# Kernel tuning notes

Hardware: AMD Instinct MI355X
Metric: run time of the kernel (lower is better)

## Reference

```python
import jax, jax.numpy as jnp
import numpy as np

GROUPS = 12
POOL = 64
TOPK = 8
LAYERS = 24
RANK = 64
HID = 1024


def setup_inputs() -> dict:
    key = jax.random.key(0)
    k1, k2, k3 = jax.random.split(key, 3)
    queries = jax.random.normal(k1, (64, 768), dtype=jnp.float32)
    keys = jax.random.normal(k2, (1, GROUPS, POOL, 768 // GROUPS), dtype=jnp.float32)
    weight_offset = jax.random.normal(
        k3, (POOL, 2, HID * RANK * LAYERS), dtype=jnp.float32
    )
    return {"queries": queries, "keys": keys, "weight_offset": weight_offset}


def reference(queries, keys, weight_offset):
    # queries: [b, g*c] -> [b, g, c]
    b = queries.shape[0]
    q = queries.reshape(b, GROUPS, -1)
    # cosine similarity against pool keys: sim [b, g, pool]
    qn = q / jnp.clip(jnp.linalg.norm(q, axis=-1, keepdims=True), 1e-8)
    kn = keys[0] / jnp.clip(jnp.linalg.norm(keys[0], axis=-1, keepdims=True), 1e-8)
    sim = jnp.einsum("bgc,gpc->bgp", qn, kn)
    # routing uses detached similarities (sim.clone().detach())
    idx_sim = jax.lax.stop_gradient(sim)
    # use_distance_weight=True path: mean over batch and groups -> [pool]
    mean_sim = jnp.mean(idx_sim, axis=(0, 1))
    dis_weight, idx_vote = jax.lax.top_k(mean_sim, TOPK)
    dis_weight = dis_weight / (dis_weight.sum() + 1e-9)
    # gather top-k low-rank factors: [k, 2, D]
    wo = weight_offset[idx_vote]
    low_rank_a = wo[:, 0, :].reshape(TOPK, LAYERS, RANK, HID)
    low_rank_b = wo[:, 1, :].reshape(TOPK, LAYERS, RANK, HID)
    # [k, L, H, H] low-rank outer products
    offset = jnp.einsum("nlrx,nlry->nlxy", low_rank_a, low_rank_b)
    # distance-weighted combine -> [L, H, H]
    weight_offset_out = jnp.einsum("n,nlxy->lxy", dis_weight, offset)
    return weight_offset_out
```

## Files before the change

### kernel.cpp

```cpp
#include <hip/hip_runtime.h>
#include <hip/hip_bf16.h>

#define GROUPS 12
#define POOL   64
#define TOPK   8
#define LAYERS 24
#define RANK   64
#define HID    1024
#define D_LR   (HID * RANK * LAYERS)
#define POOL_STRIDE (2L * D_LR)

typedef __attribute__((ext_vector_type(8))) short bf16x8;
typedef __attribute__((ext_vector_type(4))) float f32x4;

__device__ __forceinline__ unsigned bfpack2(float lo, float hi) {
    float2 t; t.x = lo; t.y = hi;
    union { __hip_bfloat162 h; unsigned u; } cv;
    cv.h = __float22bfloat162_rn(t);
    return cv.u;
}

__device__ __forceinline__ int sw_idx(int col, int chunk) {
    return chunk ^ (col & 7) ^ ((col >> 2) & 7);
}

__global__ void routing_kernel(const float* __restrict__ q,
                               const float* __restrict__ keys,
                               int* __restrict__ idx_out,
                               float* __restrict__ w_out) {
    __shared__ float invn[64][GROUPS];
    __shared__ float qbar[GROUPS][64];
    __shared__ float simg[GROUPS][64];
    const int t = threadIdx.x;

    {
        int b = t / GROUPS, g = t % GROUPS;
        const float* row = q + b * 768 + g * 64;
        float ss = 0.f;
        #pragma unroll 8
        for (int c = 0; c < 64; ++c) { float v = row[c]; ss = fmaf(v, v, ss); }
        invn[b][g] = 1.f / fmaxf(sqrtf(ss), 1e-8f);
    }
    __syncthreads();
    {
        int g = t >> 6, c = t & 63;
        float s = 0.f;
        for (int b = 0; b < 64; ++b) s = fmaf(q[b * 768 + g * 64 + c], invn[b][g], s);
        qbar[g][c] = s;
    }
    __syncthreads();
    {
        int g = t >> 6, p = t & 63;
        const float* krow = keys + (g * 64 + p) * 64;
        float ss = 0.f, dot = 0.f;
        #pragma unroll 8
        for (int c = 0; c < 64; ++c) {
            float v = krow[c];
            ss  = fmaf(v, v, ss);
            dot = fmaf(v, qbar[g][c], dot);
        }
        simg[g][p] = dot / fmaxf(sqrtf(ss), 1e-8f);
    }
    __syncthreads();
    if (t < 64) {
        float s = 0.f;
        for (int g = 0; g < GROUPS; ++g) s += simg[g][t];
        qbar[0][t] = s * (1.f / 768.f);
    }
    __syncthreads();
    if (t == 0) {
        float ms[POOL];
        for (int p = 0; p < POOL; ++p) ms[p] = qbar[0][p];
        float sum = 0.f;
        float vals[TOPK]; int ids[TOPK];
        for (int k = 0; k < TOPK; ++k) {
            float best = -3.4e38f; int bi = 0;
            for (int p = 0; p < POOL; ++p)
                if (ms[p] > best) { best = ms[p]; bi = p; }
            vals[k] = best; ids[k] = bi;
            ms[bi] = -3.4e38f; sum += best;
        }
        float inv = 1.f / (sum + 1e-9f);
        for (int k = 0; k < TOPK; ++k) { idx_out[k] = ids[k]; w_out[k] = vals[k] * inv; }
    }
}

__global__ __launch_bounds__(512, 2) void lowrank_mfma_kernel(
        const float* __restrict__ wo,
        const int*   __restrict__ idx,
        const float* __restrict__ w,
        float*       __restrict__ out)
{
    __shared__ uint4 As4[256][8];
    __shared__ uint4 Bs4[256][8];
    __shared__ int   s_idx[TOPK];
    __shared__ float s_w[TOPK];

    const int tid = threadIdx.x;
    const int b   = blockIdx.x;
    const int xcd = b & 7;
    const int i   = b >> 3;

    const int tile0 = (2 * xcd + (i >> 4)) * 16 + (i & 15);
    const int nt    = (i < 16) ? 2 : 1;
    const int tile1 = (16 + xcd) * 16 + i;

    if (tid < TOPK) { s_idx[tid] = idx[tid]; s_w[tid] = w[tid]; }
    __syncthreads();

    const int lane = tid & 63;
    const int wave = tid >> 6;
    const int wr = wave >> 2;
    const int wc = wave & 3;
    const int fr = lane & 15;
    const int kb = lane >> 4;

    const int c4 = lane;
    const int rg = wave;

    f32x4 acc[8][4];
    #pragma unroll
    for (int p = 0; p < 8; ++p)
        #pragma unroll
        for (int q2 = 0; q2 < 4; ++q2) acc[p][q2] = (f32x4){0.f, 0.f, 0.f, 0.f};

    f32x4 araw[8], braw[8];

    auto load_raw = [&](int T, int s) {
        const int l   = T >> 4;
        const int rem = T & 15;
        const int m0  = (rem >> 2) * 256;
        const int n0  = (rem & 3) * 256;
        const long base = (long)s_idx[s] * POOL_STRIDE + (long)l * (RANK * HID);
        const float* pa = wo + base + (long)(rg * 8) * HID + (m0 + c4 * 4);
        const float* pb = wo + base + D_LR + (long)(rg * 8) * HID + (n0 + c4 * 4);
        #pragma unroll
        for (int j = 0; j < 8; ++j) araw[j] = *(const f32x4*)(pa + (long)j * HID);
        #pragma unroll
        for (int j = 0; j < 8; ++j) braw[j] = *(const f32x4*)(pb + (long)j * HID);
    };

    load_raw(tile0, 0);

    for (int ti = 0; ti < nt; ++ti) {
        const int T   = (ti == 0) ? tile0 : tile1;
        const int l   = T >> 4;
        const int rem = T & 15;
        const int m0  = (rem >> 2) * 256;
        const int n0  = (rem & 3) * 256;

        for (int s = 0; s < 8; ++s) {
            const float wn = s_w[s];
            #pragma unroll
            for (int cc = 0; cc < 4; ++cc) {
                const int col = c4 * 4 + cc;
                uint4 ua, ub;
                ua.x = bfpack2(wn * araw[0][cc], wn * araw[1][cc]);
                ua.y = bfpack2(wn * araw[2][cc], wn * araw[3][cc]);
                ua.z = bfpack2(wn * araw[4][cc], wn * araw[5][cc]);
                ua.w = bfpack2(wn * araw[6][cc], wn * araw[7][cc]);
                ub.x = bfpack2(braw[0][cc], braw[1][cc]);
                ub.y = bfpack2(braw[2][cc], braw[3][cc]);
                ub.z = bfpack2(braw[4][cc], braw[5][cc]);
                ub.w = bfpack2(braw[6][cc], braw[7][cc]);
                const int cp = sw_idx(col, rg);
                As4[col][cp] = ua;
                Bs4[col][cp] = ub;
            }
            __syncthreads();

            if (s < 7)            load_raw(T, s + 1);
            else if (ti + 1 < nt) load_raw(tile1, 0);

            #pragma unroll
            for (int kk = 0; kk < 2; ++kk) {
                const int chunk = kk * 4 + kb;
                bf16x8 bfv[4];
                #pragma unroll
                for (int fj = 0; fj < 4; ++fj) {
                    const int n = wc * 64 + fj * 16 + fr;
                    bfv[fj] = *(const bf16x8*)&Bs4[n][sw_idx(n, chunk)];
                }
                #pragma unroll
                for (int fi = 0; fi < 8; ++fi) {
                    const int m = wr * 128 + fi * 16 + fr;
                    const bf16x8 af = *(const bf16x8*)&As4[m][sw_idx(m, chunk)];
                    #pragma unroll
                    for (int fj = 0; fj < 4; ++fj)
                        acc[fi][fj] = __builtin_amdgcn_mfma_f32_16x16x32_bf16(
                            af, bfv[fj], acc[fi][fj], 0, 0, 0);
                }
            }
            __syncthreads();
        }

        float* o = out + (long)l * (1024 * 1024);
        #pragma unroll
        for (int fi = 0; fi < 8; ++fi) {
            #pragma unroll
            for (int fj = 0; fj < 4; ++fj) {
                const int n = n0 + wc * 64 + fj * 16 + fr;
                #pragma unroll
                for (int v = 0; v < 4; ++v) {
                    const int m = m0 + wr * 128 + fi * 16 + kb * 4 + v;
                    o[(long)m * 1024 + n] = acc[fi][fj][v];
                }
                acc[fi][fj] = (f32x4){0.f, 0.f, 0.f, 0.f};
            }
        }
    }
}

extern "C" void kernel_launch(void* const* d_in, const int* in_sizes, int n_in,
                              void* d_out, int out_size, void* d_ws, size_t ws_size,
                              hipStream_t stream) {
    const float* q    = (const float*)d_in[0];
    const float* keys = (const float*)d_in[1];
    const float* wo   = (const float*)d_in[2];
    float* out = (float*)d_out;

    int*   idx = (int*)d_ws;
    float* w   = (float*)((char*)d_ws + 32);

    routing_kernel<<<1, 768, 0, stream>>>(q, keys, idx, w);

    lowrank_mfma_kernel<<<dim3(256, 1, 1), 512, 0, stream>>>(wo, idx, w, out);
}
```

Baseline: 80.14 us.

## Pre-convert selected low-rank factors to swizzled bf16 panels, stream via LDS loads

Adds a separate convert kernel that gathers the top-k factor slices, applies the distance weight, converts them to bf16 and writes them to a workspace in a pre-swizzled panel layout. The GEMM kernel then copies those panels straight into double-buffered LDS with global_load_lds, so the per-tile fp32 loads and register conversion are gone and the next stage's loads overlap the MFMA work. The cost is an extra kernel launch and a workspace round-trip of the bf16 panels. The new path depends on the workspace being large enough; otherwise it falls back to the old kernel.

```diff
diff --git a/kernel.cpp b/kernel.cpp
--- a/kernel.cpp
+++ b/kernel.cpp
@@ -9,6 +9,8 @@
 #define HID    1024
 #define D_LR   (HID * RANK * LAYERS)
 #define POOL_STRIDE (2L * D_LR)
+#define PAN_U4 8192
+#define WS_PAN_BYTES ((size_t)LAYERS * TOPK * 2 * PAN_U4 * 16)
 
 typedef __attribute__((ext_vector_type(8))) short bf16x8;
 typedef __attribute__((ext_vector_type(4))) float f32x4;
@@ -22,6 +24,12 @@
 
 __device__ __forceinline__ int sw_idx(int col, int chunk) {
     return chunk ^ (col & 7) ^ ((col >> 2) & 7);
+}
+
+__device__ __forceinline__ void gll16(const void* g, void* l) {
+    __builtin_amdgcn_global_load_lds(
+        (const __attribute__((address_space(1))) unsigned*)g,
+        (__attribute__((address_space(3))) unsigned*)l, 16, 0, 0);
 }
 
 __global__ void routing_kernel(const float* __restrict__ q,
@@ -85,16 +93,40 @@
     }
 }
 
-__global__ __launch_bounds__(512, 2) void lowrank_mfma_kernel(
-        const float* __restrict__ wo,
-        const int*   __restrict__ idx,
-        const float* __restrict__ w,
+__global__ __launch_bounds__(256) void convert_kernel(
+        const float* __restrict__ wo, const int* __restrict__ idx,
+        const float* __restrict__ w, uint4* __restrict__ pan) {
+    const int bid = blockIdx.x;
+    const int mat = bid & 1;
+    const int s   = (bid >> 1) & 7;
+    const int cb  = (bid >> 4) & 3;
+    const int l   = bid >> 6;
+    const int tid = threadIdx.x;
+    const int col = cb * 256 + tid;
+    const float wn = mat ? 1.0f : w[s];
+    const float* src = wo + (long)idx[s] * POOL_STRIDE + (long)mat * D_LR
+                     + (long)l * (RANK * HID) + col;
+    float v[64];
+    #pragma unroll
+    for (int r = 0; r < 64; ++r) v[r] = src[(long)r * HID] * wn;
+    uint4* dst = pan + (long)((l * 8 + s) * 2 + mat) * PAN_U4 + col * 8;
+    #pragma unroll
+    for (int qc = 0; qc < 8; ++qc) {
+        uint4 u;
+        u.x = bfpack2(v[qc*8+0], v[qc*8+1]);
+        u.y = bfpack2(v[qc*8+2], v[qc*8+3]);
+        u.z = bfpack2(v[qc*8+4], v[qc*8+5]);
+        u.w = bfpack2(v[qc*8+6], v[qc*8+7]);
+        dst[qc ^ (col & 7)] = u;
+    }
+}
+
+__global__ __launch_bounds__(512) void lowrank_mfma2_kernel(
+        const uint4* __restrict__ pan,
         float*       __restrict__ out)
 {
-    __shared__ uint4 As4[256][8];
-    __shared__ uint4 Bs4[256][8];
-    __shared__ int   s_idx[TOPK];
-    __shared__ float s_w[TOPK];
+    __shared__ uint4 As4[2][256 * 8];
+    __shared__ uint4 Bs4[2][256 * 8];
 
     const int tid = threadIdx.x;
     const int b   = blockIdx.x;
@@ -104,9 +136,6 @@
     const int tile0 = (2 * xcd + (i >> 4)) * 16 + (i & 15);
     const int nt    = (i < 16) ? 2 : 1;
     const int tile1 = (16 + xcd) * 16 + i;
-
-    if (tid < TOPK) { s_idx[tid] = idx[tid]; s_w[tid] = w[tid]; }
-    __syncthreads();
 
     const int lane = tid & 63;
     const int wave = tid >> 6;
@@ -115,40 +144,127 @@
     const int fr = lane & 15;
     const int kb = lane >> 4;
 
-    const int c4 = lane;
-    const int rg = wave;
-
     f32x4 acc[8][4];
     #pragma unroll
     for (int p = 0; p < 8; ++p)
         #pragma unroll
         for (int q2 = 0; q2 < 4; ++q2) acc[p][q2] = (f32x4){0.f, 0.f, 0.f, 0.f};
 
-    f32x4 araw[8], braw[8];
-
-    auto load_raw = [&](int T, int s) {
+    auto stage = [&](int buf, int T, int s) {
         const int l   = T >> 4;
         const int rem = T & 15;
         const int m0  = (rem >> 2) * 256;
         const int n0  = (rem & 3) * 256;
-        const long base = (long)s_idx[s] * POOL_STRIDE + (long)l * (RANK * HID);
-        const float* pa = wo + base + (long)(rg * 8) * HID + (m0 + c4 * 4);
-        const float* pb = wo + base + D_LR + (long)(rg * 8) * HID + (n0 + c4 * 4);
-        #pragma unroll
-        for (int j = 0; j < 8; ++j) araw[j] = *(const f32x4*)(pa + (long)j * HID);
-        #pragma unroll
-        for (int j = 0; j < 8; ++j) braw[j] = *(const f32x4*)(pb + (long)j * HID);
+        const uint4* pa = pan + (long)((l * 8 + s) * 2 + 0) * PAN_U4 + m0 * 8;
+        const uint4* pb = pan + (long)((l * 8 + s) * 2 + 1) * PAN_U4 + n0 * 8;
+        #pragma unroll
+        for (int t2 = 0; t2 < 4; ++t2) {
+            gll16(pa + t2 * 512 + tid, &As4[buf][t2 * 512 + wave * 64]);
+            gll16(pb + t2 * 512 + tid, &Bs4[buf][t2 * 512 + wave * 64]);
+        }
     };
 
-    load_raw(tile0, 0);
-
-    for (int ti = 0; ti < nt; ++ti) {
-        const int T   = (ti == 0) ? tile0 : tile1;
+    auto epilogue = [&](int T) {
         const int l   = T >> 4;
         const int rem = T & 15;
         const int m0  = (rem >> 2) * 256;
         const int n0  = (rem & 3) * 256;
-
+        float* o = out + (long)l * (1024 * 1024);
+        #pragma unroll
+        for (int fi = 0; fi < 8; ++fi)
+            #pragma unroll
+            for (int fj = 0; fj < 4; ++fj) {
+                const int n = n0 + wc * 64 + fj * 16 + fr;
+                #pragma unroll
+                for (int v = 0; v < 4; ++v) {
+                    const int m = m0 + wr * 128 + fi * 16 + kb * 4 + v;
+                    o[(long)m * 1024 + n] = acc[fi][fj][v];
+                }
+                acc[fi][fj] = (f32x4){0.f, 0.f, 0.f, 0.f};
+            }
+    };
+
+    stage(0, tile0, 0);
+    const int ms_total = nt * 8;
+    for (int ms = 0; ms < ms_total; ++ms) {
+        const int cur = ms & 1;
+        __syncthreads();
+        if (ms + 1 < ms_total)
+            stage(cur ^ 1, (ms + 1 < 8) ? tile0 : tile1, (ms + 1) & 7);
+
+        #pragma unroll
+        for (int kk = 0; kk < 2; ++kk) {
+            const int chunk = kk * 4 + kb;
+            bf16x8 bfv[4];
+            #pragma unroll
+            for (int fj = 0; fj < 4; ++fj) {
+                const int n = wc * 64 + fj * 16 + fr;
+                bfv[fj] = *(const bf16x8*)&Bs4[cur][n * 8 + (chunk ^ (n & 7))];
+            }
+            #pragma unroll
+            for (int fi = 0; fi < 8; ++fi) {
+                const int m = wr * 128 + fi * 16 + fr;
+                const bf16x8 af = *(const bf16x8*)&As4[cur][m * 8 + (chunk ^ (m & 7))];
+                #pragma unroll
+                for (int fj = 0; fj < 4; ++fj)
+                    acc[fi][fj] = __builtin_amdgcn_mfma_f32_16x16x32_bf16(
+                        af, bfv[fj], acc[fi][fj], 0, 0, 0);
+            }
+        }
+        if ((ms & 7) == 7) epilogue(ms < 8 ? tile0 : tile1);
+    }
+}
+
+__global__ __launch_bounds__(512, 2) void lowrank_mfma_kernel(
+        const float* __restrict__ wo, const int* __restrict__ idx,
+        const float* __restrict__ w, float* __restrict__ out)
+{
+    __shared__ uint4 As4[256][8];
+    __shared__ uint4 Bs4[256][8];
+    __shared__ int   s_idx[TOPK];
+    __shared__ float s_w[TOPK];
+
+    const int tid = threadIdx.x;
+    const int b   = blockIdx.x;
+    const int xcd = b & 7;
+    const int i   = b >> 3;
+    const int tile0 = (2 * xcd + (i >> 4)) * 16 + (i & 15);
+    const int nt    = (i < 16) ? 2 : 1;
+    const int tile1 = (16 + xcd) * 16 + i;
+
+    if (tid < TOPK) { s_idx[tid] = idx[tid]; s_w[tid] = w[tid]; }
+    __syncthreads();
+
+    const int lane = tid & 63;
+    const int wave = tid >> 6;
+    const int wr = wave >> 2, wc = wave & 3;
+    const int fr = lane & 15, kb = lane >> 4;
+    const int c4 = lane, rg = wave;
+
+    f32x4 acc[8][4];
+    #pragma unroll
+    for (int p = 0; p < 8; ++p)
+        #pragma unroll
+        for (int q2 = 0; q2 < 4; ++q2) acc[p][q2] = (f32x4){0.f, 0.f, 0.f, 0.f};
+
+    f32x4 araw[8], braw[8];
+    auto load_raw = [&](int T, int s) {
+        const int l = T >> 4, rem = T & 15;
+        const int m0 = (rem >> 2) * 256, n0 = (rem & 3) * 256;
+        const long base = (long)s_idx[s] * POOL_STRIDE + (long)l * (RANK * HID);
+        const float* pa = wo + base + (long)(rg * 8) * HID + (m0 + c4 * 4);
+        const float* pb = wo + base + D_LR + (long)(rg * 8) * HID + (n0 + c4 * 4);
+        #pragma unroll
+        for (int j = 0; j < 8; ++j) araw[j] = *(const f32x4*)(pa + (long)j * HID);
+        #pragma unroll
+        for (int j = 0; j < 8; ++j) braw[j] = *(const f32x4*)(pb + (long)j * HID);
+    };
+
+    load_raw(tile0, 0);
+    for (int ti = 0; ti < nt; ++ti) {
+        const int T = (ti == 0) ? tile0 : tile1;
+        const int l = T >> 4, rem = T & 15;
+        const int m0 = (rem >> 2) * 256, n0 = (rem & 3) * 256;
         for (int s = 0; s < 8; ++s) {
             const float wn = s_w[s];
             #pragma unroll
@@ -168,10 +284,8 @@
                 Bs4[col][cp] = ub;
             }
             __syncthreads();
-
             if (s < 7)            load_raw(T, s + 1);
             else if (ti + 1 < nt) load_raw(tile1, 0);
-
             #pragma unroll
             for (int kk = 0; kk < 2; ++kk) {
                 const int chunk = kk * 4 + kb;
@@ -193,10 +307,9 @@
             }
             __syncthreads();
         }
-
         float* o = out + (long)l * (1024 * 1024);
         #pragma unroll
-        for (int fi = 0; fi < 8; ++fi) {
+        for (int fi = 0; fi < 8; ++fi)
             #pragma unroll
             for (int fj = 0; fj < 4; ++fj) {
                 const int n = n0 + wc * 64 + fj * 16 + fr;
@@ -207,7 +320,6 @@
                 }
                 acc[fi][fj] = (f32x4){0.f, 0.f, 0.f, 0.f};
             }
-        }
     }
 }
 
@@ -221,8 +333,14 @@
 
     int*   idx = (int*)d_ws;
     float* w   = (float*)((char*)d_ws + 32);
+    uint4* pan = (uint4*)((char*)d_ws + 1024);
 
     routing_kernel<<<1, 768, 0, stream>>>(q, keys, idx, w);
 
-    lowrank_mfma_kernel<<<dim3(256, 1, 1), 512, 0, stream>>>(wo, idx, w, out);
-}
+    if (ws_size >= 1024 + WS_PAN_BYTES) {
+        convert_kernel<<<dim3(1536, 1, 1), 256, 0, stream>>>(wo, idx, w, pan);
+        lowrank_mfma2_kernel<<<dim3(256, 1, 1), 512, 0, stream>>>(pan, out);
+    } else {
+        lowrank_mfma_kernel<<<dim3(256, 1, 1), 512, 0, stream>>>(wo, idx, w, out);
+    }
+}
```

Measured after the change: 124.0 us. 54.7% more time.
